# Kernel optimization log

Hardware: AMD Instinct MI355X
Metric: run time of the kernel (lower is better)

The kernel has to match this reference:

```python
import jax, jax.numpy as jnp
import numpy as np

N_NODES = 50000
N_EDGES = 600000
DIN, DH, DOUT = 128, 256, 128
BN_EPS = 1e-5
LRELU_SLOPE = 0.01


def setup_inputs() -> dict:
    key = jax.random.key(0)
    ks = jax.random.split(key, 16)
    rn = lambda k, s, sc=0.05: jax.random.normal(k, s, dtype=jnp.float32) * sc
    return {
        'nodes': jax.random.normal(ks[0], (N_NODES, DIN), dtype=jnp.float32),
        'src': jax.random.randint(ks[1], (N_EDGES,), 0, N_NODES, dtype=jnp.int32),
        'dst': jax.random.randint(ks[2], (N_EDGES,), 0, N_NODES, dtype=jnp.int32),
        # FeedForward params
        'Wf1': rn(ks[3], (DIN, DH)), 'bf1': jnp.zeros((DH,), jnp.float32),
        'gf1': jnp.ones((DH,), jnp.float32), 'bef1': jnp.zeros((DH,), jnp.float32),
        'Wf2': rn(ks[4], (DH, DIN)), 'bf2': jnp.zeros((DIN,), jnp.float32),
        'gf2': jnp.ones((DIN,), jnp.float32), 'bef2': jnp.zeros((DIN,), jnp.float32),
        # SAGEConv 1 (in->hidden)
        'Ws1': rn(ks[5], (DIN, DH)), 'Wn1': rn(ks[6], (DIN, DH)), 'b1': jnp.zeros((DH,), jnp.float32),
        'gs1': jnp.ones((DH,), jnp.float32), 'bs1': jnp.zeros((DH,), jnp.float32),
        # SAGEConv 2 (hidden->out)
        'Ws2': rn(ks[7], (DH, DOUT)), 'Wn2': rn(ks[8], (DH, DOUT)), 'b2': jnp.zeros((DOUT,), jnp.float32),
        'gs2': jnp.ones((DOUT,), jnp.float32), 'bs2': jnp.zeros((DOUT,), jnp.float32),
    }


def _bn(x, gamma, beta):
    # BatchNorm1d, training mode: batch stats over node dim, biased variance
    mu = jnp.mean(x, axis=0)
    var = jnp.mean(jnp.square(x - mu), axis=0)
    return (x - mu) * jax.lax.rsqrt(var + BN_EPS) * gamma + beta


def _sage_mean(x, src, dst, Wself, Wneigh, bias):
    # DGL SAGEConv('mean'): out = x@Wself + mean_{src->dst}(x[src])@Wneigh + bias
    n = x.shape[0]
    deg = jax.ops.segment_sum(jnp.ones_like(src, dtype=x.dtype), dst, num_segments=n)
    agg = jax.ops.segment_sum(x[src], dst, num_segments=n)  # [N, d] irregular scatter-add
    h_neigh = agg / jnp.maximum(deg, 1.0)[:, None]
    return x @ Wself + h_neigh @ Wneigh + bias


def reference(nodes, src, dst, Wf1, bf1, gf1, bef1, Wf2, bf2, gf2, bef2,
              Ws1, Wn1, b1, gs1, bs1, Ws2, Wn2, b2, gs2, bs2):
    # FeedForward (dropout=0 -> identity)
    h = jax.nn.relu(_bn(nodes @ Wf1 + bf1, gf1, bef1))
    h = jax.nn.relu(_bn(h @ Wf2 + bf2, gf2, bef2))
    # SAGE layer 1
    h1 = _sage_mean(h, src, dst, Ws1, Wn1, b1)
    h1 = jax.nn.leaky_relu(_bn(h1, gs1, bs1), LRELU_SLOPE)
    # SAGE layer 2
    h2 = _sage_mean(h1, src, dst, Ws2, Wn2, b2)
    return jax.nn.leaky_relu(_bn(h2, gs2, bs2), LRELU_SLOPE)
```

## Files before the change

### kernel.cpp

```cpp
#include <hip/hip_runtime.h>

#define DIN 128
#define BN_EPS 1e-5f

typedef __attribute__((ext_vector_type(8))) short bf16x8;
typedef __attribute__((ext_vector_type(8))) unsigned short us8;
typedef __attribute__((ext_vector_type(4))) float f32x4;

__device__ __forceinline__ ushort f2bf(float f) {
    unsigned u = __float_as_uint(f);
    u += 0x7fffu + ((u >> 16) & 1u);
    return (ushort)(u >> 16);
}
__device__ __forceinline__ float bf2f(ushort h) {
    return __uint_as_float(((unsigned)h) << 16);
}

template<int KC, int NT, int LOGNG, int STATS, int BNIN>
__global__ __launch_bounds__(256) void gemm_lds(
    const ushort* __restrict__ A, const ushort* __restrict__ BT,
    ushort* __restrict__ C, int mStrips, int N,
    float* __restrict__ gsums, float* __restrict__ gsqs,
    const float* __restrict__ isums, const float* __restrict__ isqs,
    const float* __restrict__ igam, const float* __restrict__ ibet,
    float invM, float negSlope)
{
    constexpr int K = KC * 32;
    constexpr int CPR = KC * 4;
    constexpr int LOGCPR = (KC == 4) ? 4 : 5;
    constexpr int LPL = KC / 4;
    __shared__ ushort abuf[2][16 * K];

    int tid = threadIdx.x;
    int lane = tid & 63;
    int w = tid >> 6;
    int cl = lane & 15, q = lane >> 4;
    int grp = blockIdx.x & ((1 << LOGNG) - 1);
    int s0 = blockIdx.x >> LOGNG;
    int TT = gridDim.x >> LOGNG;
    int colBase = grp * (4 * 16 * NT) + w * (16 * NT);
    int chBase = w * (16 * KC);

    bf16x8 bf[NT][KC];
    #pragma unroll
    for (int nt = 0; nt < NT; nt++) {
        const ushort* bp = BT + (long)(colBase + nt * 16 + cl) * K + q * 8;
        #pragma unroll
        for (int kc = 0; kc < KC; kc++)
            bf[nt][kc] = *(const bf16x8*)(bp + kc * 32);
    }

    float sc8[8], sh8[8];
    if (BNIN) {
        int cb = ((chBase + lane) & (CPR - 1)) * 8;
        #pragma unroll
        for (int e = 0; e < 8; e++) {
            float mean = isums[cb + e] * invM;
            float var = isqs[cb + e] * invM - mean * mean;
            float s = igam[cb + e] * rsqrtf(var + BN_EPS);
            sc8[e] = s;
            sh8[e] = ibet[cb + e] - mean * s;
        }
    }

    float ssum[NT], ssq[NT];
    #pragma unroll
    for (int nt = 0; nt < NT; nt++) { ssum[nt] = 0.f; ssq[nt] = 0.f; }

    auto stage_load = [&](us8 (&stg)[LPL], int strip) {
        const ushort* As = A + (long)strip * 16 * K;
        #pragma unroll
        for (int u = 0; u < LPL; u++)
            stg[u] = *(const us8*)(As + (chBase + u * 64 + lane) * 8);
    };
    auto stage_write = [&](int buf, us8 (&stg)[LPL]) {
        #pragma unroll
        for (int u = 0; u < LPL; u++) {
            int ch = chBase + u * 64 + lane;
            int r = ch >> LOGCPR;
            int c = ch & (CPR - 1);
            us8 v = stg[u];
            if (BNIN) {
                us8 o;
                #pragma unroll
                for (int e = 0; e < 8; e++) {
                    float f = bf2f(v[e]) * sc8[e] + sh8[e];
                    f = (f > 0.f) ? f : f * negSlope;
                    o[e] = f2bf(f);
                }
                v = o;
            }
            *(us8*)(abuf[buf] + (((r << LOGCPR) + (c ^ (r & 7))) * 8)) = v;
        }
    };

    us8 stgA[LPL], stgB[LPL];
    int s = s0;
    stage_load(stgA, s);
    if (s + TT < mStrips) stage_load(stgB, s + TT);
    stage_write(0, stgA);
    if (s + 2 * TT < mStrips) stage_load(stgA, s + 2 * TT);
    __syncthreads();
    int cur = 0;

#define GEMM_STEP(STG)                                                                  \
    {                                                                                   \
        bf16x8 af[KC];                                                                  \
        _Pragma("unroll")                                                               \
        for (int kc = 0; kc < KC; kc++)                                                 \
            af[kc] = *(const bf16x8*)(abuf[cur] +                                       \
                     (((cl << LOGCPR) + ((kc * 4 + q) ^ (cl & 7))) * 8));               \
        if (s + TT < mStrips) stage_write(cur ^ 1, STG);                                \
        if (s + 3 * TT < mStrips) stage_load(STG, s + 3 * TT);                          \
        f32x4 acc[NT] = {};                                                             \
        _Pragma("unroll")                                                               \
        for (int kc = 0; kc < KC; kc++)                                                 \
            _Pragma("unroll")                                                           \
            for (int nt = 0; nt < NT; nt++)                                             \
                acc[nt] = __builtin_amdgcn_mfma_f32_16x16x32_bf16(af[kc], bf[nt][kc],   \
                                                                  acc[nt], 0, 0, 0);    \
        int rowBase = s * 16;                                                           \
        _Pragma("unroll")                                                               \
        for (int nt = 0; nt < NT; nt++) {                                               \
            _Pragma("unroll")                                                           \
            for (int r = 0; r < 4; r++) {                                               \
                float v = acc[nt][r];                                                   \
                long row = rowBase + q * 4 + r;                                         \
                C[row * N + colBase + nt * 16 + cl] = f2bf(v);                          \
                if (STATS) { ssum[nt] += v; ssq[nt] += v * v; }                         \
            }                                                                           \
        }                                                                               \
        __syncthreads();                                                                \
        s += TT; cur ^= 1;                                                              \
    }

    while (true) {
        GEMM_STEP(stgB);
        if (s >= mStrips) break;
        GEMM_STEP(stgA);
        if (s >= mStrips) break;
    }
#undef GEMM_STEP

    if (STATS) {
        #pragma unroll
        for (int nt = 0; nt < NT; nt++) {
            ssum[nt] += __shfl_xor(ssum[nt], 16, 64);
            ssum[nt] += __shfl_xor(ssum[nt], 32, 64);
            ssq[nt]  += __shfl_xor(ssq[nt], 16, 64);
            ssq[nt]  += __shfl_xor(ssq[nt], 32, 64);
        }
        if (q == 0) {
            #pragma unroll
            for (int nt = 0; nt < NT; nt++) {
                atomicAdd(&gsums[colBase + nt * 16 + cl], ssum[nt]);
                atomicAdd(&gsqs[colBase + nt * 16 + cl], ssq[nt]);
            }
        }
    }
}

__global__ __launch_bounds__(256) void setup_all(
    const float* __restrict__ nodes, ushort* __restrict__ Xbf, int nConv4, int nbConv,
    const float* __restrict__ W0, const float* __restrict__ W1,
    const float* __restrict__ W2, const float* __restrict__ W3,
    const float* __restrict__ W4, const float* __restrict__ W5,
    ushort* __restrict__ WT,
    int* __restrict__ zeroInts, int nZero4, int nbZero,
    float* __restrict__ stats)
{
    int b = blockIdx.x;
    int tid = threadIdx.x;
    if (b < nbConv) {
        int t = b * 256 + tid;
        if (t < nConv4) {
            float4 v = *(const float4*)&nodes[(long)t * 4];
            ushort4 o; o.x = f2bf(v.x); o.y = f2bf(v.y); o.z = f2bf(v.z); o.w = f2bf(v.w);
            *(ushort4*)&Xbf[(long)t * 4] = o;
        }
        return;
    }
    b -= nbConv;
    if (b < 768) {
        int seg = b >> 7;
        const float* W; int logK, dstBase, stride, kOff;
        switch (seg) {
            case 0: W = W0; logK = 7; dstBase = 0;      stride = 128; kOff = 0;   break;
            case 1: W = W1; logK = 8; dstBase = 32768;  stride = 256; kOff = 0;   break;
            case 2: W = W2; logK = 7; dstBase = 65536;  stride = 256; kOff = 0;   break;
            case 3: W = W3; logK = 7; dstBase = 65536;  stride = 256; kOff = 128; break;
            case 4: W = W4; logK = 8; dstBase = 131072; stride = 256; kOff = 0;   break;
            default:W = W5; logK = 8; dstBase = 163840; stride = 256; kOff = 0;   break;
        }
        int t = (b & 127) * 256 + tid;
        int N = 32768 >> logK;
        int k = t & ((1 << logK) - 1);
        int n = t >> logK;
        WT[(long)dstBase + (long)n * stride + kOff + k] = f2bf(W[(long)k * N + n]);
        return;
    }
    b -= 768;
    if (b < nbZero) {
        int t = b * 256 + tid;
        if (t < nZero4) *(int4*)&zeroInts[(long)t * 4] = make_int4(0, 0, 0, 0);
        return;
    }
    b -= nbZero;
    int t = b * 256 + tid;
    if (t < 512) *(float4*)&stats[(long)t * 4] = make_float4(0, 0, 0, 0);
}

template<int LOGN>
__global__ __launch_bounds__(256) void bnact_bf16(
    const ushort* __restrict__ X,
    const float* __restrict__ sums, const float* __restrict__ sqs,
    const float* __restrict__ gamma, const float* __restrict__ beta, float invM,
    ushort* __restrict__ O, int nRows, int outStride, float negSlope)
{
    constexpr int NCH = 1 << LOGN;
    __shared__ float ssc[NCH], ssh[NCH];
    int tid = threadIdx.x;
    if (tid < NCH) {
        float mean = sums[tid] * invM;
        float var = sqs[tid] * invM - mean * mean;
        float sc = gamma[tid] * rsqrtf(var + BN_EPS);
        ssc[tid] = sc;
        ssh[tid] = beta[tid] - mean * sc;
    }
    __syncthreads();
    int cb = (tid * 8) & (NCH - 1);
    float4 sA = *(const float4*)&ssc[cb];
    float4 sB = *(const float4*)&ssc[cb + 4];
    float4 hA = *(const float4*)&ssh[cb];
    float4 hB = *(const float4*)&ssh[cb + 4];
    const int rpb = (256 * 8) >> LOGN;
    int r0 = blockIdx.x * rpb + ((tid * 8) >> LOGN);
    int rstride = gridDim.x * rpb;
    for (int row = r0; row < nRows; row += rstride) {
        us8 v = *(const us8*)&X[(long)row * NCH + cb];
        float f0 = bf2f(v[0]) * sA.x + hA.x; f0 = (f0 > 0.f) ? f0 : f0 * negSlope;
        float f1 = bf2f(v[1]) * sA.y + hA.y; f1 = (f1 > 0.f) ? f1 : f1 * negSlope;
        float f2 = bf2f(v[2]) * sA.z + hA.z; f2 = (f2 > 0.f) ? f2 : f2 * negSlope;
        float f3 = bf2f(v[3]) * sA.w + hA.w; f3 = (f3 > 0.f) ? f3 : f3 * negSlope;
        float f4 = bf2f(v[4]) * sB.x + hB.x; f4 = (f4 > 0.f) ? f4 : f4 * negSlope;
        float f5 = bf2f(v[5]) * sB.y + hB.y; f5 = (f5 > 0.f) ? f5 : f5 * negSlope;
        float f6 = bf2f(v[6]) * sB.z + hB.z; f6 = (f6 > 0.f) ? f6 : f6 * negSlope;
        float f7 = bf2f(v[7]) * sB.w + hB.w; f7 = (f7 > 0.f) ? f7 : f7 * negSlope;
        us8 o;
        o[0] = f2bf(f0); o[1] = f2bf(f1); o[2] = f2bf(f2); o[3] = f2bf(f3);
        o[4] = f2bf(f4); o[5] = f2bf(f5); o[6] = f2bf(f6); o[7] = f2bf(f7);
        *(us8*)&O[(long)row * outStride + cb] = o;
    }
}

__global__ __launch_bounds__(256) void bnact_f32(
    float* __restrict__ X,
    const float* __restrict__ sums, const float* __restrict__ sqs,
    const float* __restrict__ gamma, const float* __restrict__ beta, float invM,
    int nRows, float negSlope)
{
    __shared__ float ssc[128], ssh[128];
    int tid = threadIdx.x;
    if (tid < 128) {
        float mean = sums[tid] * invM;
        float var = sqs[tid] * invM - mean * mean;
        float sc = gamma[tid] * rsqrtf(var + BN_EPS);
        ssc[tid] = sc;
        ssh[tid] = beta[tid] - mean * sc;
    }
    __syncthreads();
    int cb = (tid * 4) & 127;
    float4 sc = *(const float4*)&ssc[cb];
    float4 sh = *(const float4*)&ssh[cb];
    int r0 = blockIdx.x * 8 + ((tid * 4) >> 7);
    int rstride = gridDim.x * 8;
    for (int row = r0; row < nRows; row += rstride) {
        float4 v = *(const float4*)&X[(long)row * 128 + cb];
        float a = v.x * sc.x + sh.x; a = (a > 0.f) ? a : a * negSlope;
        float b = v.y * sc.y + sh.y; b = (b > 0.f) ? b : b * negSlope;
        float d = v.z * sc.z + sh.z; d = (d > 0.f) ? d : d * negSlope;
        float e = v.w * sc.w + sh.w; e = (e > 0.f) ? e : e * negSlope;
        *(float4*)&X[(long)row * 128 + cb] = make_float4(a, b, d, e);
    }
}

__global__ __launch_bounds__(256) void colstats128(
    const float* __restrict__ X, float* __restrict__ sums, float* __restrict__ sqs, int M)
{
    __shared__ float ss[128], sq[128];
    int tid = threadIdx.x;
    if (tid < 128) { ss[tid] = 0.f; sq[tid] = 0.f; }
    __syncthreads();
    int cg = tid & 31;
    int worker = (blockIdx.x << 3) | (tid >> 5);
    int totalW = gridDim.x << 3;
    float4 s4 = make_float4(0, 0, 0, 0), q4 = make_float4(0, 0, 0, 0);
    for (int r = worker; r < M; r += totalW) {
        float4 v = *(const float4*)&X[(long)r * 128 + cg * 4];
        s4.x += v.x; s4.y += v.y; s4.z += v.z; s4.w += v.w;
        q4.x += v.x * v.x; q4.y += v.y * v.y; q4.z += v.z * v.z; q4.w += v.w * v.w;
    }
    atomicAdd(&ss[cg * 4 + 0], s4.x); atomicAdd(&sq[cg * 4 + 0], q4.x);
    atomicAdd(&ss[cg * 4 + 1], s4.y); atomicAdd(&sq[cg * 4 + 1], q4.y);
    atomicAdd(&ss[cg * 4 + 2], s4.z); atomicAdd(&sq[cg * 4 + 2], q4.z);
    atomicAdd(&ss[cg * 4 + 3], s4.w); atomicAdd(&sq[cg * 4 + 3], q4.w);
    __syncthreads();
    if (tid < 128) { atomicAdd(&sums[tid], ss[tid]); atomicAdd(&sqs[tid], sq[tid]); }
}

__global__ void degcount_kernel(const int* __restrict__ dst, int* __restrict__ degi, int E)
{
    int i = blockIdx.x * blockDim.x + threadIdx.x;
    if (i < E) atomicAdd(&degi[dst[i]], 1);
}

__global__ __launch_bounds__(256) void scan_block_sums(const int* __restrict__ degi,
                                                       int* __restrict__ partial, int n)
{
    __shared__ int s[256];
    int i = blockIdx.x * 256 + threadIdx.x;
    s[threadIdx.x] = (i < n) ? degi[i] : 0;
    __syncthreads();
    for (int off = 128; off > 0; off >>= 1) {
        if (threadIdx.x < off) s[threadIdx.x] += s[threadIdx.x + off];
        __syncthreads();
    }
    if (threadIdx.x == 0) partial[blockIdx.x] = s[0];
}

__global__ __launch_bounds__(256) void scan_final(const int* __restrict__ degi,
                                                  const int* __restrict__ partial,
                                                  int* __restrict__ rowstart, int n, int nb)
{
    __shared__ int s[256];
    __shared__ int ps[256];
    int tid = threadIdx.x;
    ps[tid] = (tid < nb && tid < (int)blockIdx.x) ? partial[tid] : 0;
    __syncthreads();
    for (int off = 128; off > 0; off >>= 1) {
        if (tid < off) ps[tid] += ps[tid + off];
        __syncthreads();
    }
    int offset = ps[0];
    int i = blockIdx.x * 256 + tid;
    int v = (i < n) ? degi[i] : 0;
    s[tid] = v;
    __syncthreads();
    for (int off = 1; off < 256; off <<= 1) {
        int t = (tid >= off) ? s[tid - off] : 0;
        __syncthreads();
        s[tid] += t;
        __syncthreads();
    }
    if (i < n) rowstart[i] = offset + s[tid] - v;
}

__global__ void fillcsr_kernel(const int* __restrict__ src, const int* __restrict__ dst,
                               const int* __restrict__ rowstart, int* __restrict__ cursor,
                               int* __restrict__ csr, int E)
{
    int i = blockIdx.x * blockDim.x + threadIdx.x;
    if (i < E) {
        int d = dst[i];
        int p = atomicAdd(&cursor[d], 1);
        csr[rowstart[d] + p] = src[i];
    }
}

__device__ __forceinline__ void acc8(float acc[8], us8 v) {
    #pragma unroll
    for (int e = 0; e < 8; e++) acc[e] += bf2f(v[e]);
}

__global__ __launch_bounds__(256) void gather16_bf(
    const ushort* __restrict__ X, const int* __restrict__ rowstart,
    const int* __restrict__ degi, const int* __restrict__ csr,
    ushort* __restrict__ O, int nN)
{
    int wv = (blockIdx.x * blockDim.x + threadIdx.x) >> 6;
    int lane = threadIdx.x & 63;
    if (wv >= nN) return;
    int g = lane >> 4;
    int sc = lane & 15;
    int start = rowstart[wv], d = degi[wv];
    const ushort* Xc = X + sc * 8;
    float acc[8] = {};
    if (d > 0) {
        int dm = (d < 64) ? d : 64;
        int idx_l = csr[start + ((lane < dm) ? lane : (dm - 1))];
        int j = 0;
        for (; j + 8 <= dm; j += 8) {
            int i0 = __shfl(idx_l, j + g, 64);
            int i1 = __shfl(idx_l, j + 4 + g, 64);
            us8 v0 = *(const us8*)(Xc + (long)i0 * 256);
            us8 v1 = *(const us8*)(Xc + (long)i1 * 256);
            acc8(acc, v0);
            acc8(acc, v1);
        }
        if (j + 4 <= dm) {
            int i0 = __shfl(idx_l, j + g, 64);
            us8 v0 = *(const us8*)(Xc + (long)i0 * 256);
            acc8(acc, v0);
            j += 4;
        }
        int rem = dm - j;
        if (rem > 0) {
            int sl = j + ((g < rem) ? g : (rem - 1));
            int i0 = __shfl(idx_l, sl, 64);
            if (g < rem) {
                us8 v0 = *(const us8*)(Xc + (long)i0 * 256);
                acc8(acc, v0);
            }
        }
        for (int jj = 64; jj < d; jj += 4) {
            if (jj + g < d) {
                int i0 = csr[start + jj + g];
                us8 v0 = *(const us8*)(Xc + (long)i0 * 256);
                acc8(acc, v0);
            }
        }
    }
    #pragma unroll
    for (int e = 0; e < 8; e++) {
        acc[e] += __shfl_xor(acc[e], 16, 64);
        acc[e] += __shfl_xor(acc[e], 32, 64);
    }
    if (g == 0) {
        float inv = 1.f / fmaxf((float)d, 1.f);
        us8 o;
        #pragma unroll
        for (int e = 0; e < 8; e++) o[e] = f2bf(acc[e] * inv);
        *(us8*)(O + (long)wv * 256 + sc * 8) = o;
    }
}

__global__ __launch_bounds__(256) void gather16_fuse(
    const ushort* __restrict__ Z, const int* __restrict__ rowstart,
    const int* __restrict__ degi, const int* __restrict__ csr,
    float* __restrict__ O, int nN)
{
    int wv = (blockIdx.x * blockDim.x + threadIdx.x) >> 6;
    int lane = threadIdx.x & 63;
    if (wv >= nN) return;
    int g = lane >> 4;
    int sc = lane & 15;
    int start = rowstart[wv], d = degi[wv];
    const ushort* Zc = Z + sc * 8;
    us8 selfv = *(const us8*)(Zc + (long)wv * 256 + 128);
    float acc[8] = {};
    if (d > 0) {
        int dm = (d < 64) ? d : 64;
        int idx_l = csr[start + ((lane < dm) ? lane : (dm - 1))];
        int j = 0;
        for (; j + 8 <= dm; j += 8) {
            int i0 = __shfl(idx_l, j + g, 64);
            int i1 = __shfl(idx_l, j + 4 + g, 64);
            us8 v0 = *(const us8*)(Zc + (long)i0 * 256);
            us8 v1 = *(const us8*)(Zc + (long)i1 * 256);
            acc8(acc, v0);
            acc8(acc, v1);
        }
        if (j + 4 <= dm) {
            int i0 = __shfl(idx_l, j + g, 64);
            us8 v0 = *(const us8*)(Zc + (long)i0 * 256);
            acc8(acc, v0);
            j += 4;
        }
        int rem = dm - j;
        if (rem > 0) {
            int sl = j + ((g < rem) ? g : (rem - 1));
            int i0 = __shfl(idx_l, sl, 64);
            if (g < rem) {
                us8 v0 = *(const us8*)(Zc + (long)i0 * 256);
                acc8(acc, v0);
            }
        }
        for (int jj = 64; jj < d; jj += 4) {
            if (jj + g < d) {
                int i0 = csr[start + jj + g];
                us8 v0 = *(const us8*)(Zc + (long)i0 * 256);
                acc8(acc, v0);
            }
        }
    }
    #pragma unroll
    for (int e = 0; e < 8; e++) {
        acc[e] += __shfl_xor(acc[e], 16, 64);
        acc[e] += __shfl_xor(acc[e], 32, 64);
    }
    if (g == 0) {
        float inv = 1.f / fmaxf((float)d, 1.f);
        float r[8];
        #pragma unroll
        for (int e = 0; e < 8; e++) r[e] = acc[e] * inv + bf2f(selfv[e]);
        float* op = O + (long)wv * 128 + sc * 8;
        *(float4*)op = make_float4(r[0], r[1], r[2], r[3]);
        *(float4*)(op + 4) = make_float4(r[4], r[5], r[6], r[7]);
    }
}

extern "C" void kernel_launch(void* const* d_in, const int* in_sizes, int n_in,
                              void* d_out, int out_size, void* d_ws, size_t ws_size,
                              hipStream_t stream)
{
    const float* nodes = (const float*)d_in[0];
    const int*   src   = (const int*)d_in[1];
    const int*   dst   = (const int*)d_in[2];
    const float* Wf1   = (const float*)d_in[3];
    const float* gf1   = (const float*)d_in[5];
    const float* bef1  = (const float*)d_in[6];
    const float* Wf2   = (const float*)d_in[7];
    const float* gf2   = (const float*)d_in[9];
    const float* bef2  = (const float*)d_in[10];
    const float* Ws1   = (const float*)d_in[11];
    const float* Wn1   = (const float*)d_in[12];
    const float* gs1   = (const float*)d_in[14];
    const float* bs1   = (const float*)d_in[15];
    const float* Ws2   = (const float*)d_in[16];
    const float* Wn2   = (const float*)d_in[17];
    const float* gs2   = (const float*)d_in[19];
    const float* bs2   = (const float*)d_in[20];

    int nN = in_sizes[0] / DIN;
    int nE = in_sizes[1];
    float* out = (float*)d_out;
    int mStrips = nN / 16;
    float invM = 1.0f / nN;

    ushort* PRE = (ushort*)d_ws;
    ushort* BF1 = PRE + (size_t)nN * 256;
    ushort* BF2 = BF1 + (size_t)nN * 256;
    float* stats = (float*)(BF2 + (size_t)nN * 256);
    float* scale = stats + 2048;
    float* shift = scale + 256;
    ushort* WT   = (ushort*)(shift + 256);
    int* degi     = (int*)(WT + 196608);
    int* cursor   = degi + nN;
    int* rowstart = cursor + nN;
    int* partial  = rowstart + nN;
    int* csr      = partial + 256;

    ushort* Wf1T = WT;
    ushort* Wf2T = WT + 32768;
    ushort* Wc1T = WT + 65536;
    ushort* Wc2T = WT + 131072;

    dim3 blk(256);
    auto cdiv = [](int a, int b) { return (a + b - 1) / b; };
    int nScanBlocks = cdiv(nN, 256);

    int nConv4 = nN * DIN / 4;
    int nbConv = cdiv(nConv4, 256);
    int nZero4 = (2 * nN) / 4;
    int nbZero = cdiv(nZero4, 256);
    setup_all<<<dim3(nbConv + 768 + nbZero + 2), blk, 0, stream>>>(
        nodes, BF1, nConv4, nbConv,
        Wf1, Wf2, Ws1, Wn1, Wn2, Ws2, WT,
        degi, nZero4, nbZero, stats);

    degcount_kernel<<<dim3(cdiv(nE, 256)), blk, 0, stream>>>(dst, degi, nE);
    scan_block_sums<<<dim3(nScanBlocks), blk, 0, stream>>>(degi, partial, nN);
    scan_final<<<dim3(nScanBlocks), blk, 0, stream>>>(degi, partial, rowstart, nN, nScanBlocks);
    fillcsr_kernel<<<dim3(cdiv(nE, 256)), blk, 0, stream>>>(src, dst, rowstart, cursor, csr, nE);

    gemm_lds<4, 4, 0, 1, 0><<<dim3(512), blk, 0, stream>>>(
        BF1, Wf1T, PRE, mStrips, 256, stats, stats + 256,
        nullptr, nullptr, nullptr, nullptr, 0.f, 0.f);

    gemm_lds<8, 2, 0, 1, 1><<<dim3(512), blk, 0, stream>>>(
        PRE, Wf2T, BF1, mStrips, 128, stats + 512, stats + 768,
        stats, stats + 256, gf1, bef1, invM, 0.0f);

    bnact_bf16<7><<<dim3(2048), blk, 0, stream>>>(BF1, stats + 512, stats + 768, gf2, bef2, invM,
                                                  BF2, nN, 256, 0.0f);

    gather16_bf<<<dim3(cdiv(nN * 64, 256)), blk, 0, stream>>>(BF2, rowstart, degi, csr, BF2 + 128, nN);

    gemm_lds<8, 4, 0, 1, 0><<<dim3(512), blk, 0, stream>>>(
        BF2, Wc1T, PRE, mStrips, 256, stats + 1024, stats + 1280,
        nullptr, nullptr, nullptr, nullptr, 0.f, 0.f);

    gemm_lds<8, 2, 1, 0, 1><<<dim3(512), blk, 0, stream>>>(
        PRE, Wc2T, BF2, mStrips, 256, nullptr, nullptr,
        stats + 1024, stats + 1280, gs1, bs1, invM, 0.01f);

    gather16_fuse<<<dim3(cdiv(nN * 64, 256)), blk, 0, stream>>>(BF2, rowstart, degi, csr, out, nN);

    colstats128<<<dim3(120), blk, 0, stream>>>(out, stats + 1536, stats + 1792, nN);
    bnact_f32<<<dim3(2048), blk, 0, stream>>>(out, stats + 1536, stats + 1792, gs2, bs2, invM,
                                              nN, 0.01f);
}
```

Measured before the change: 355.5 us.

## Fuse second FeedForward BN+ReLU into neighbor gather and SAGE-1 GEMM load

Drops the standalone bf16 BN+ReLU pass. The gather kernel now applies BN+ReLU on the fly to raw 128-wide rows it fetches and writes only the aggregated half. The first SAGE GEMM gets a new load mode that reads the self half from the raw pre-activation buffer (applying BN+ReLU while staging) and the neighbor half from a separate aggregate buffer. This removes one full read/write pass over the node features and halves the gather row stride, at the cost of extra per-element BN math in the gather loop and more complex addressing in the GEMM load.

New measurement: 351.1 us. No clear change (-1.3%).

```diff
diff --git a/kernel.cpp b/kernel.cpp
--- a/kernel.cpp
+++ b/kernel.cpp
@@ -23,7 +23,8 @@
     float* __restrict__ gsums, float* __restrict__ gsqs,
     const float* __restrict__ isums, const float* __restrict__ isqs,
     const float* __restrict__ igam, const float* __restrict__ ibet,
-    float invM, float negSlope)
+    float invM, float negSlope,
+    const ushort* __restrict__ A2)
 {
     constexpr int K = KC * 32;
     constexpr int CPR = KC * 4;
@@ -51,7 +52,9 @@
     }
 
     float sc8[8], sh8[8];
-    if (BNIN) {
+    const ushort* dsrc = A;
+    int dcol = 0;
+    if (BNIN == 1) {
         int cb = ((chBase + lane) & (CPR - 1)) * 8;
         #pragma unroll
         for (int e = 0; e < 8; e++) {
@@ -61,6 +64,24 @@
             sc8[e] = s;
             sh8[e] = ibet[cb + e] - mean * s;
         }
+    } else if (BNIN == 2) {
+        int c = (chBase + lane) & (CPR - 1);
+        dsrc = (c < 16) ? A : A2;
+        dcol = (c & 15) * 8;
+        if (c < 16) {
+            int cb = c * 8;
+            #pragma unroll
+            for (int e = 0; e < 8; e++) {
+                float mean = isums[cb + e] * invM;
+                float var = isqs[cb + e] * invM - mean * mean;
+                float s = igam[cb + e] * rsqrtf(var + BN_EPS);
+                sc8[e] = s;
+                sh8[e] = ibet[cb + e] - mean * s;
+            }
+        } else {
+            #pragma unroll
+            for (int e = 0; e < 8; e++) { sc8[e] = 1.0f; sh8[e] = 0.0f; }
+        }
     }
 
     float ssum[NT], ssq[NT];
@@ -68,10 +89,18 @@
     for (int nt = 0; nt < NT; nt++) { ssum[nt] = 0.f; ssq[nt] = 0.f; }
 
     auto stage_load = [&](us8 (&stg)[LPL], int strip) {
-        const ushort* As = A + (long)strip * 16 * K;
-        #pragma unroll
-        for (int u = 0; u < LPL; u++)
-            stg[u] = *(const us8*)(As + (chBase + u * 64 + lane) * 8);
+        if (BNIN == 2) {
+            #pragma unroll
+            for (int u = 0; u < LPL; u++) {
+                int r = (chBase + u * 64 + lane) >> LOGCPR;
+                stg[u] = *(const us8*)(dsrc + ((long)(strip * 16 + r)) * 128 + dcol);
+            }
+        } else {
+            const ushort* As = A + (long)strip * 16 * K;
+            #pragma unroll
+            for (int u = 0; u < LPL; u++)
+                stg[u] = *(const us8*)(As + (chBase + u * 64 + lane) * 8);
+        }
     };
     auto stage_write = [&](int buf, us8 (&stg)[LPL]) {
         #pragma unroll
@@ -80,7 +109,7 @@
             int r = ch >> LOGCPR;
             int c = ch & (CPR - 1);
             us8 v = stg[u];
-            if (BNIN) {
+            if (BNIN != 0) {
                 us8 o;
                 #pragma unroll
                 for (int e = 0; e < 8; e++) {
@@ -210,49 +239,6 @@
     if (t < 512) *(float4*)&stats[(long)t * 4] = make_float4(0, 0, 0, 0);
 }
 
-template<int LOGN>
-__global__ __launch_bounds__(256) void bnact_bf16(
-    const ushort* __restrict__ X,
-    const float* __restrict__ sums, const float* __restrict__ sqs,
-    const float* __restrict__ gamma, const float* __restrict__ beta, float invM,
-    ushort* __restrict__ O, int nRows, int outStride, float negSlope)
-{
-    constexpr int NCH = 1 << LOGN;
-    __shared__ float ssc[NCH], ssh[NCH];
-    int tid = threadIdx.x;
-    if (tid < NCH) {
-        float mean = sums[tid] * invM;
-        float var = sqs[tid] * invM - mean * mean;
-        float sc = gamma[tid] * rsqrtf(var + BN_EPS);
-        ssc[tid] = sc;
-        ssh[tid] = beta[tid] - mean * sc;
-    }
-    __syncthreads();
-    int cb = (tid * 8) & (NCH - 1);
-    float4 sA = *(const float4*)&ssc[cb];
-    float4 sB = *(const float4*)&ssc[cb + 4];
-    float4 hA = *(const float4*)&ssh[cb];
-    float4 hB = *(const float4*)&ssh[cb + 4];
-    const int rpb = (256 * 8) >> LOGN;
-    int r0 = blockIdx.x * rpb + ((tid * 8) >> LOGN);
-    int rstride = gridDim.x * rpb;
-    for (int row = r0; row < nRows; row += rstride) {
-        us8 v = *(const us8*)&X[(long)row * NCH + cb];
-        float f0 = bf2f(v[0]) * sA.x + hA.x; f0 = (f0 > 0.f) ? f0 : f0 * negSlope;
-        float f1 = bf2f(v[1]) * sA.y + hA.y; f1 = (f1 > 0.f) ? f1 : f1 * negSlope;
-        float f2 = bf2f(v[2]) * sA.z + hA.z; f2 = (f2 > 0.f) ? f2 : f2 * negSlope;
-        float f3 = bf2f(v[3]) * sA.w + hA.w; f3 = (f3 > 0.f) ? f3 : f3 * negSlope;
-        float f4 = bf2f(v[4]) * sB.x + hB.x; f4 = (f4 > 0.f) ? f4 : f4 * negSlope;
-        float f5 = bf2f(v[5]) * sB.y + hB.y; f5 = (f5 > 0.f) ? f5 : f5 * negSlope;
-        float f6 = bf2f(v[6]) * sB.z + hB.z; f6 = (f6 > 0.f) ? f6 : f6 * negSlope;
-        float f7 = bf2f(v[7]) * sB.w + hB.w; f7 = (f7 > 0.f) ? f7 : f7 * negSlope;
-        us8 o;
-        o[0] = f2bf(f0); o[1] = f2bf(f1); o[2] = f2bf(f2); o[3] = f2bf(f3);
-        o[4] = f2bf(f4); o[5] = f2bf(f5); o[6] = f2bf(f6); o[7] = f2bf(f7);
-        *(us8*)&O[(long)row * outStride + cb] = o;
-    }
-}
-
 __global__ __launch_bounds__(256) void bnact_f32(
     float* __restrict__ X,
     const float* __restrict__ sums, const float* __restrict__ sqs,
@@ -367,24 +353,38 @@
     }
 }
 
-__device__ __forceinline__ void acc8(float acc[8], us8 v) {
-    #pragma unroll
-    for (int e = 0; e < 8; e++) acc[e] += bf2f(v[e]);
-}
-
-__global__ __launch_bounds__(256) void gather16_bf(
+__global__ __launch_bounds__(256) void gather16_bn(
     const ushort* __restrict__ X, const int* __restrict__ rowstart,
     const int* __restrict__ degi, const int* __restrict__ csr,
-    ushort* __restrict__ O, int nN)
+    ushort* __restrict__ AGG, int nN,
+    const float* __restrict__ isums, const float* __restrict__ isqs,
+    const float* __restrict__ igam, const float* __restrict__ ibet, float invM)
 {
     int wv = (blockIdx.x * blockDim.x + threadIdx.x) >> 6;
     int lane = threadIdx.x & 63;
     if (wv >= nN) return;
     int g = lane >> 4;
     int sc = lane & 15;
+    float sc8[8], sh8[8];
+    {
+        int cb = sc * 8;
+        #pragma unroll
+        for (int e = 0; e < 8; e++) {
+            float mean = isums[cb + e] * invM;
+            float var = isqs[cb + e] * invM - mean * mean;
+            float s = igam[cb + e] * rsqrtf(var + BN_EPS);
+            sc8[e] = s;
+            sh8[e] = ibet[cb + e] - mean * s;
+        }
+    }
     int start = rowstart[wv], d = degi[wv];
     const ushort* Xc = X + sc * 8;
     float acc[8] = {};
+    auto accbn8 = [&](us8 v) {
+        #pragma unroll
+        for (int e = 0; e < 8; e++)
+            acc[e] += fmaxf(bf2f(v[e]) * sc8[e] + sh8[e], 0.f);
+    };
     if (d > 0) {
         int dm = (d < 64) ? d : 64;
         int idx_l = csr[start + ((lane < dm) ? lane : (dm - 1))];
@@ -392,15 +392,15 @@
         for (; j + 8 <= dm; j += 8) {
             int i0 = __shfl(idx_l, j + g, 64);
             int i1 = __shfl(idx_l, j + 4 + g, 64);
-            us8 v0 = *(const us8*)(Xc + (long)i0 * 256);
-            us8 v1 = *(const us8*)(Xc + (long)i1 * 256);
-            acc8(acc, v0);
-            acc8(acc, v1);
+            us8 v0 = *(const us8*)(Xc + (long)i0 * 128);
+            us8 v1 = *(const us8*)(Xc + (long)i1 * 128);
+            accbn8(v0);
+            accbn8(v1);
         }
         if (j + 4 <= dm) {
             int i0 = __shfl(idx_l, j + g, 64);
-            us8 v0 = *(const us8*)(Xc + (long)i0 * 256);
-            acc8(acc, v0);
+            us8 v0 = *(const us8*)(Xc + (long)i0 * 128);
+            accbn8(v0);
             j += 4;
         }
         int rem = dm - j;
@@ -408,15 +408,15 @@
             int sl = j + ((g < rem) ? g : (rem - 1));
             int i0 = __shfl(idx_l, sl, 64);
             if (g < rem) {
-                us8 v0 = *(const us8*)(Xc + (long)i0 * 256);
-                acc8(acc, v0);
+                us8 v0 = *(const us8*)(Xc + (long)i0 * 128);
+                accbn8(v0);
             }
         }
         for (int jj = 64; jj < d; jj += 4) {
             if (jj + g < d) {
                 int i0 = csr[start + jj + g];
-                us8 v0 = *(const us8*)(Xc + (long)i0 * 256);
-                acc8(acc, v0);
+                us8 v0 = *(const us8*)(Xc + (long)i0 * 128);
+                accbn8(v0);
             }
         }
     }
@@ -430,8 +430,13 @@
         us8 o;
         #pragma unroll
         for (int e = 0; e < 8; e++) o[e] = f2bf(acc[e] * inv);
-        *(us8*)(O + (long)wv * 256 + sc * 8) = o;
-    }
+        *(us8*)(AGG + (long)wv * 128 + sc * 8) = o;
+    }
+}
+
+__device__ __forceinline__ void acc8(float acc[8], us8 v) {
+    #pragma unroll
+    for (int e = 0; e < 8; e++) acc[e] += bf2f(v[e]);
 }
 
 __global__ __launch_bounds__(256) void gather16_fuse(
@@ -544,6 +549,7 @@
     ushort* Wf2T = WT + 32768;
     ushort* Wc1T = WT + 65536;
     ushort* Wc2T = WT + 131072;
+    ushort* AGG  = BF2;
 
     dim3 blk(256);
     auto cdiv = [](int a, int b) { return (a + b - 1) / b; };
@@ -565,24 +571,23 @@
 
     gemm_lds<4, 4, 0, 1, 0><<<dim3(512), blk, 0, stream>>>(
         BF1, Wf1T, PRE, mStrips, 256, stats, stats + 256,
-        nullptr, nullptr, nullptr, nullptr, 0.f, 0.f);
+        nullptr, nullptr, nullptr, nullptr, 0.f, 0.f, nullptr);
 
     gemm_lds<8, 2, 0, 1, 1><<<dim3(512), blk, 0, stream>>>(
         PRE, Wf2T, BF1, mStrips, 128, stats + 512, stats + 768,
-        stats, stats + 256, gf1, bef1, invM, 0.0f);
-
-    bnact_bf16<7><<<dim3(2048), blk, 0, stream>>>(BF1, stats + 512, stats + 768, gf2, bef2, invM,
-                                                  BF2, nN, 256, 0.0f);
-
-    gather16_bf<<<dim3(cdiv(nN * 64, 256)), blk, 0, stream>>>(BF2, rowstart, degi, csr, BF2 + 128, nN);
-
-    gemm_lds<8, 4, 0, 1, 0><<<dim3(512), blk, 0, stream>>>(
-        BF2, Wc1T, PRE, mStrips, 256, stats + 1024, stats + 1280,
-        nullptr, nullptr, nullptr, nullptr, 0.f, 0.f);
+        stats, stats + 256, gf1, bef1, invM, 0.0f, nullptr);
+
+    gather16_bn<<<dim3(cdiv(nN * 64, 256)), blk, 0, stream>>>(
+        BF1, rowstart, degi, csr, AGG, nN,
+        stats + 512, stats + 768, gf2, bef2, invM);
+
+    gemm_lds<8, 4, 0, 1, 2><<<dim3(512), blk, 0, stream>>>(
+        BF1, Wc1T, PRE, mStrips, 256, stats + 1024, stats + 1280,
+        stats + 512, stats + 768, gf2, bef2, invM, 0.0f, AGG);
 
     gemm_lds<8, 2, 1, 0, 1><<<dim3(512), blk, 0, stream>>>(
         PRE, Wc2T, BF2, mStrips, 256, nullptr, nullptr,
-        stats + 1024, stats + 1280, gs1, bs1, invM, 0.01f);
+        stats + 1024, stats + 1280, gs1, bs1, invM, 0.01f, nullptr);
 
     gather16_fuse<<<dim3(cdiv(nN * 64, 256)), blk, 0, stream>>>(BF2, rowstart, degi, csr, out, nN);
 
```
